# Kernel optimization log

Measured on AMD Instinct MI355X. Metric: run time of the kernel, lower is better.

## Reference

```python
import jax, jax.numpy as jnp
import numpy as np

NT, NF, CIN, COUT = 1_500_000, 500_000, 32, 32
BN_EPS = 1e-5


def setup_inputs() -> dict:
    key = jax.random.key(0)
    k1, k2, k3 = jax.random.split(key, 3)
    input_texture = jax.random.normal(k1, (NT, CIN), dtype=jnp.float32)
    # barycentric coefficients: nonnegative, rows sum to 1
    b = jax.random.uniform(k2, (NT, 3), dtype=jnp.float32) + 1e-3
    bary_coeff = b / b.sum(axis=1, keepdims=True)
    # 3 texture samples per facet (sum == NT)
    num_texture = jnp.full((NF,), 3, dtype=jnp.int32)
    # xavier-normal init for [Cout, Cin, 3] kernel
    fan = CIN * 3 + COUT * 3
    std = float(np.sqrt(2.0 / fan))
    weights = jax.random.normal(k3, (COUT, CIN, 3), dtype=jnp.float32) * std
    bias = jnp.zeros((1, COUT), dtype=jnp.float32)
    gamma = jnp.ones((COUT,), dtype=jnp.float32)
    beta = jnp.zeros((COUT,), dtype=jnp.float32)
    return {"input_texture": input_texture, "bary_coeff": bary_coeff,
            "num_texture": num_texture, "weights": weights, "bias": bias,
            "gamma": gamma, "beta": beta}


def reference(input_texture, bary_coeff, num_texture, weights, bias, gamma, beta):
    nf = num_texture.shape[0]
    nt = input_texture.shape[0]
    # segment id for each ragged texture sample (original op uses cumsum offsets)
    seg = jnp.repeat(jnp.arange(nf), num_texture, total_repeat_length=nt)
    # per-sample contribution: y[t,o] = sum_{c,k} x[t,c] * b[t,k] * W[o,c,k]
    y = jnp.einsum('tc,tk,ock->to', input_texture, bary_coeff, weights)
    # facet2facet averages over the samples of each facet
    s = jax.ops.segment_sum(y, seg, num_segments=nf)  # [Nf, Cout]
    cnt = jnp.maximum(num_texture.astype(y.dtype), 1)[:, None]
    out = s / cnt
    out = out + bias          # bias add
    out = jax.nn.relu(out)    # activation
    # BatchNorm1d in training mode: batch statistics over the facet dim
    mean = out.mean(axis=0)
    var = out.var(axis=0)
    out = (out - mean) * jax.lax.rsqrt(var + BN_EPS) * gamma + beta
    return out
```

## Files before the change

kernel.cpp:

```cpp
#include <hip/hip_runtime.h>
#include <hip/hip_bf16.h>
#include <stdint.h>

typedef __attribute__((ext_vector_type(4))) float fv4;
typedef __attribute__((ext_vector_type(4))) short sv4;
typedef __attribute__((ext_vector_type(8))) short sv8;

#define SCHUNK 2048
#define NIT 4
#define SPAN (64 * NIT)
#define PZB 108

static __device__ __forceinline__ short f2bf(float f) {
  __hip_bfloat16 h = __float2bfloat16(f);
  union { __hip_bfloat16 h; short s; } u; u.h = h;
  return u.s;
}

__global__ __launch_bounds__(256) void scan1(const int* __restrict__ num, int nf,
                                             int* __restrict__ bsum) {
  __shared__ int sd[256];
  int b = blockIdx.x, tid = threadIdx.x;
  int base = b * SCHUNK + tid * 8;
  int s = 0;
#pragma unroll
  for (int j = 0; j < 8; ++j) { int i = base + j; if (i < nf) s += num[i]; }
  sd[tid] = s; __syncthreads();
  for (int st = 128; st > 0; st >>= 1) {
    if (tid < st) sd[tid] += sd[tid + st];
    __syncthreads();
  }
  if (tid == 0) bsum[b] = sd[0];
}

__global__ __launch_bounds__(256) void scan2(int* __restrict__ bsum, int nb) {
  __shared__ int sd[256];
  int tid = threadIdx.x;
  int v = (tid < nb) ? bsum[tid] : 0;
  sd[tid] = v; __syncthreads();
  for (int off = 1; off < 256; off <<= 1) {
    int t = (tid >= off) ? sd[tid - off] : 0;
    __syncthreads();
    sd[tid] += t;
    __syncthreads();
  }
  if (tid < nb) bsum[tid] = sd[tid] - v;
}

__global__ __launch_bounds__(256) void scan3(const int* __restrict__ num, int nf,
                                             const int* __restrict__ bsum,
                                             int* __restrict__ offsets) {
  __shared__ int sc_[256];
  int b = blockIdx.x, tid = threadIdx.x;
  int base = b * SCHUNK + tid * 8;
  int loc[8]; int s = 0;
#pragma unroll
  for (int j = 0; j < 8; ++j) {
    loc[j] = (base + j < nf) ? num[base + j] : 0;
    s += loc[j];
  }
  sc_[tid] = s; __syncthreads();
  for (int off = 1; off < 256; off <<= 1) {
    int t = (tid >= off) ? sc_[tid - off] : 0;
    __syncthreads();
    sc_[tid] += t;
    __syncthreads();
  }
  int run = bsum[b] + sc_[tid] - s;
#pragma unroll
  for (int j = 0; j < 8; ++j) {
    if (base + j < nf) offsets[base + j] = run;
    run += loc[j];
  }
  if (b == gridDim.x - 1 && tid == 255) offsets[nf] = run;
}

__global__ __launch_bounds__(256) void k_main(
    const float* __restrict__ x, const float* __restrict__ bary,
    const float* __restrict__ W, const float* __restrict__ bias,
    const int* __restrict__ offsets, float* __restrict__ out,
    float* __restrict__ partials, int nf, int nt, int nw)
{
  __shared__ short W2[32 * PZB];
  __shared__ short Z[4 * 16 * PZB];

  const int tid = threadIdx.x;
  const int lane = tid & 63;
  const int wv = tid >> 6;
  short* Zw = &Z[wv * 16 * PZB];

  for (int idx = tid; idx < 3072; idx += 256) {
    int o = idx / 96;
    int ck = idx - o * 96;
    int k = ck >> 5, c = ck & 31;
    W2[o * PZB + ck] = f2bf(W[o * 96 + c * 3 + k]);
  }
  __syncthreads();

  const int fl = lane >> 2;
  const int cb = (lane & 3) * 8;
  const int rowl = lane & 15;
  const int grp = lane >> 4;
  const int blk0 = blockIdx.x * SPAN;

  float bo0 = bias[rowl];
  float bo1 = bias[16 + rowl];
  float s1l = 0.f, s1h = 0.f, s2l = 0.f, s2h = 0.f;

  for (int t = 0; t < NIT; ++t) {
    const int f0t = blk0 + t * 64 + wv * 16;
    const int f = f0t + fl;
    const int fa = f < nf ? f : nf;
    const int fb = (f + 1) < nf ? (f + 1) : nf;

    const int st = offsets[fa];
    const int en = offsets[fb];
    const int s3 = 3 * f;
    const int sbase = (f < nf && s3 + 3 <= nt) ? s3 : 0;
    const float* xp0 = x + (size_t)(sbase + 0) * 32 + cb;
    const float* xp1 = x + (size_t)(sbase + 1) * 32 + cb;
    const float* xp2 = x + (size_t)(sbase + 2) * 32 + cb;
    fv4 x0a = *(const fv4*)(xp0), x0b = *(const fv4*)(xp0 + 4);
    fv4 x1a = *(const fv4*)(xp1), x1b = *(const fv4*)(xp1 + 4);
    fv4 x2a = *(const fv4*)(xp2), x2b = *(const fv4*)(xp2 + 4);
    const float* bp0 = bary + (size_t)(sbase + 0) * 3;
    const float* bp1 = bary + (size_t)(sbase + 1) * 3;
    const float* bp2 = bary + (size_t)(sbase + 2) * 3;
    float b00 = bp0[0], b01 = bp0[1], b02 = bp0[2];
    float b10 = bp1[0], b11 = bp1[1], b12 = bp1[2];
    float b20 = bp2[0], b21 = bp2[1], b22 = bp2[2];

    const int nm_my = en - st;

    float z0[8], z1[8], z2[8];
#pragma unroll
    for (int j = 0; j < 8; ++j) { z0[j] = 0.f; z1[j] = 0.f; z2[j] = 0.f; }

    if (nm_my == 3 && st == s3) {
#pragma unroll
      for (int j = 0; j < 4; ++j) {
        z0[j]     += x0a[j] * b00; z1[j]     += x0a[j] * b01; z2[j]     += x0a[j] * b02;
        z0[4 + j] += x0b[j] * b00; z1[4 + j] += x0b[j] * b01; z2[4 + j] += x0b[j] * b02;
      }
#pragma unroll
      for (int j = 0; j < 4; ++j) {
        z0[j]     += x1a[j] * b10; z1[j]     += x1a[j] * b11; z2[j]     += x1a[j] * b12;
        z0[4 + j] += x1b[j] * b10; z1[4 + j] += x1b[j] * b11; z2[4 + j] += x1b[j] * b12;
      }
#pragma unroll
      for (int j = 0; j < 4; ++j) {
        z0[j]     += x2a[j] * b20; z1[j]     += x2a[j] * b21; z2[j]     += x2a[j] * b22;
        z0[4 + j] += x2b[j] * b20; z1[4 + j] += x2b[j] * b21; z2[4 + j] += x2b[j] * b22;
      }
    } else {
      for (int t2 = st; t2 < en; ++t2) {
        const float* xp = x + (size_t)t2 * 32 + cb;
        fv4 xa = *(const fv4*)(xp);
        fv4 xb = *(const fv4*)(xp + 4);
        const float* bp = bary + (size_t)t2 * 3;
        float b0 = bp[0], b1 = bp[1], b2 = bp[2];
#pragma unroll
        for (int j = 0; j < 4; ++j) {
          z0[j]     += xa[j] * b0; z1[j]     += xa[j] * b1; z2[j]     += xa[j] * b2;
          z0[4 + j] += xb[j] * b0; z1[4 + j] += xb[j] * b1; z2[4 + j] += xb[j] * b2;
        }
      }
    }

    short* zr = &Zw[fl * PZB + cb];
#pragma unroll
    for (int g = 0; g < 2; ++g) {
      sv4 p0, p1, p2;
#pragma unroll
      for (int j = 0; j < 4; ++j) {
        p0[j] = f2bf(z0[g * 4 + j]);
        p1[j] = f2bf(z1[g * 4 + j]);
        p2[j] = f2bf(z2[g * 4 + j]);
      }
      *(sv4*)(zr + g * 4)      = p0;
      *(sv4*)(zr + 32 + g * 4) = p1;
      *(sv4*)(zr + 64 + g * 4) = p2;
    }
    __builtin_amdgcn_wave_barrier();

    fv4 acc0 = (fv4){0.f, 0.f, 0.f, 0.f};
    fv4 acc1 = (fv4){0.f, 0.f, 0.f, 0.f};
#pragma unroll
    for (int kb = 0; kb < 3; ++kb) {
      const int cko = kb * 32 + grp * 4;
      sv8 bfr0, bfr1, afr;
      {
        const short* wr = &W2[rowl * PZB + cko];
        sv4 lo = *(const sv4*)(wr), hi = *(const sv4*)(wr + 16);
#pragma unroll
        for (int j = 0; j < 4; ++j) { bfr0[j] = lo[j]; bfr0[4 + j] = hi[j]; }
      }
      {
        const short* wr = &W2[(16 + rowl) * PZB + cko];
        sv4 lo = *(const sv4*)(wr), hi = *(const sv4*)(wr + 16);
#pragma unroll
        for (int j = 0; j < 4; ++j) { bfr1[j] = lo[j]; bfr1[4 + j] = hi[j]; }
      }
      {
        const short* zr2 = &Zw[rowl * PZB + cko];
        sv4 lo = *(const sv4*)(zr2), hi = *(const sv4*)(zr2 + 16);
#pragma unroll
        for (int j = 0; j < 4; ++j) { afr[j] = lo[j]; afr[4 + j] = hi[j]; }
      }
      acc0 = __builtin_amdgcn_mfma_f32_16x16x32_bf16(afr, bfr0, acc0, 0, 0, 0);
      acc1 = __builtin_amdgcn_mfma_f32_16x16x32_bf16(afr, bfr1, acc1, 0, 0, 0);
    }

#pragma unroll
    for (int r = 0; r < 4; ++r) {
      int row = grp * 4 + r;
      int fr = f0t + row;
      int nm = __shfl(nm_my, row * 4, 64);
      float inv = 1.0f / (float)(nm > 1 ? nm : 1);
      if (fr < nf) {
        float v0 = fmaxf(acc0[r] * inv + bo0, 0.f);
        float v1 = fmaxf(acc1[r] * inv + bo1, 0.f);
        out[fr * 32 + rowl]      = v0;
        out[fr * 32 + 16 + rowl] = v1;
        s1l += v0; s2l += v0 * v0;
        s1h += v1; s2h += v1 * v1;
      }
    }
    __builtin_amdgcn_wave_barrier();
  }

  s1l += __shfl_xor(s1l, 16, 64); s1l += __shfl_xor(s1l, 32, 64);
  s1h += __shfl_xor(s1h, 16, 64); s1h += __shfl_xor(s1h, 32, 64);
  s2l += __shfl_xor(s2l, 16, 64); s2l += __shfl_xor(s2l, 32, 64);
  s2h += __shfl_xor(s2h, 16, 64); s2h += __shfl_xor(s2h, 32, 64);
  if (grp == 0) {
    int w = blockIdx.x * 4 + wv;
    partials[(long)(rowl)      * nw + w] = s1l;
    partials[(long)(16 + rowl) * nw + w] = s1h;
    partials[(long)(32 + rowl) * nw + w] = s2l;
    partials[(long)(48 + rowl) * nw + w] = s2h;
  }
}

__global__ __launch_bounds__(256) void k_reduce(const float* __restrict__ partials,
                                                int nw, float* __restrict__ stats) {
  __shared__ float sd[256];
  int c = blockIdx.x;
  const float* p = partials + (long)c * nw;
  float s = 0.f;
  for (int i = threadIdx.x; i < nw; i += 256) s += p[i];
  sd[threadIdx.x] = s; __syncthreads();
  for (int st = 128; st > 0; st >>= 1) {
    if (threadIdx.x < st) sd[threadIdx.x] += sd[threadIdx.x + st];
    __syncthreads();
  }
  if (threadIdx.x == 0) stats[c] = sd[0];
}

__global__ __launch_bounds__(256) void k_bn(float* __restrict__ out,
                                            const float* __restrict__ stats,
                                            const float* __restrict__ gamma,
                                            const float* __restrict__ beta, int nf) {
  __shared__ float sc[32], sh[32];
  if (threadIdx.x < 32) {
    int o = threadIdx.x;
    float inv_n = 1.0f / (float)nf;
    float mean = stats[o] * inv_n;
    float var = stats[32 + o] * inv_n - mean * mean;
    float rstd = rsqrtf(var + 1e-5f);
    float g = gamma[o] * rstd;
    sc[o] = g;
    sh[o] = beta[o] - mean * g;
  }
  __syncthreads();
  long total4 = (long)nf * 8;
  long idx0 = (long)blockIdx.x * 256 + threadIdx.x;
  int ob = ((int)idx0 & 7) * 4;
  fv4 scv = *(const fv4*)&sc[ob];
  fv4 shv = *(const fv4*)&sh[ob];
  for (long idx = idx0; idx < total4; idx += (long)gridDim.x * 256) {
    fv4 v = *((const fv4*)out + idx);
    v = v * scv + shv;
    *((fv4*)out + idx) = v;
  }
}

extern "C" void kernel_launch(void* const* d_in, const int* in_sizes, int n_in,
                              void* d_out, int out_size, void* d_ws, size_t ws_size,
                              hipStream_t stream) {
  const float* x     = (const float*)d_in[0];
  const float* bary  = (const float*)d_in[1];
  const int*   numt  = (const int*)d_in[2];
  const float* W     = (const float*)d_in[3];
  const float* bias  = (const float*)d_in[4];
  const float* gamma = (const float*)d_in[5];
  const float* beta  = (const float*)d_in[6];
  float* out = (float*)d_out;

  const int nf   = in_sizes[2];
  const int nt   = in_sizes[0] / 32;
  const int nblk = (nf + SPAN - 1) / SPAN;
  const int nw   = nblk * 4;
  const int nbS  = (nf + SCHUNK - 1) / SCHUNK;

  char* w = (char*)d_ws;
  int* offsets = (int*)w;
  size_t off1 = (4UL * (size_t)(nf + 1) + 255) & ~255UL;
  int* bsum = (int*)(w + off1);
  size_t off2 = (off1 + 4UL * (size_t)nbS + 255) & ~255UL;
  float* partials = (float*)(w + off2);
  size_t off3 = (off2 + 4UL * 64UL * (size_t)nw + 255) & ~255UL;
  float* stats = (float*)(w + off3);

  scan1<<<nbS, 256, 0, stream>>>(numt, nf, bsum);
  scan2<<<1, 256, 0, stream>>>(bsum, nbS);
  scan3<<<nbS, 256, 0, stream>>>(numt, nf, bsum, offsets);
  k_main<<<nblk, 256, 0, stream>>>(x, bary, W, bias, offsets, out, partials, nf, nt, nw);
  k_reduce<<<64, 256, 0, stream>>>(partials, nw, stats);
  k_bn<<<2048, 256, 0, stream>>>(out, stats, gamma, beta, nf);
}
```

Baseline: 97.81 us.

## Double-buffer global loads across iterations in k_main via register sets

Restructures the per-wave loop so the global loads of x, bary and offsets for the next 64-facet tile are issued into a second register set before the current tile is computed. This software pipelining is meant to hide global memory latency behind the FMA, LDS and MFMA work of the previous tile. It roughly doubles the live registers for loaded data, which may lower occupancy, and the compiler may already have been overlapping these loads.

```diff
diff --git a/kernel.cpp b/kernel.cpp
--- a/kernel.cpp
+++ b/kernel.cpp
@@ -75,6 +75,130 @@
   if (b == gridDim.x - 1 && tid == 255) offsets[nf] = run;
 }
 
+#define DECL_SET(S) \
+  int st_##S, en_##S; \
+  fv4 x0a_##S, x0b_##S, x1a_##S, x1b_##S, x2a_##S, x2b_##S; \
+  float b00_##S, b01_##S, b02_##S, b10_##S, b11_##S, b12_##S, b20_##S, b21_##S, b22_##S;
+
+#define LOAD_SET(S, T) do { \
+  const int f_ = blk0 + (T) * 64 + wv * 16 + fl; \
+  const int fa_ = f_ < nf ? f_ : nf; \
+  const int fb_ = (f_ + 1) < nf ? (f_ + 1) : nf; \
+  st_##S = offsets[fa_]; \
+  en_##S = offsets[fb_]; \
+  const int s3_ = 3 * f_; \
+  const int sbase_ = (f_ < nf && s3_ + 3 <= nt) ? s3_ : 0; \
+  const float* xp0_ = x + (size_t)(sbase_ + 0) * 32 + cb; \
+  const float* xp1_ = x + (size_t)(sbase_ + 1) * 32 + cb; \
+  const float* xp2_ = x + (size_t)(sbase_ + 2) * 32 + cb; \
+  x0a_##S = *(const fv4*)(xp0_); x0b_##S = *(const fv4*)(xp0_ + 4); \
+  x1a_##S = *(const fv4*)(xp1_); x1b_##S = *(const fv4*)(xp1_ + 4); \
+  x2a_##S = *(const fv4*)(xp2_); x2b_##S = *(const fv4*)(xp2_ + 4); \
+  const float* bp0_ = bary + (size_t)(sbase_ + 0) * 3; \
+  const float* bp1_ = bary + (size_t)(sbase_ + 1) * 3; \
+  const float* bp2_ = bary + (size_t)(sbase_ + 2) * 3; \
+  b00_##S = bp0_[0]; b01_##S = bp0_[1]; b02_##S = bp0_[2]; \
+  b10_##S = bp1_[0]; b11_##S = bp1_[1]; b12_##S = bp1_[2]; \
+  b20_##S = bp2_[0]; b21_##S = bp2_[1]; b22_##S = bp2_[2]; \
+} while (0)
+
+#define COMPUTE_SET(S, T) do { \
+  const int f0t = blk0 + (T) * 64 + wv * 16; \
+  const int f_ = f0t + fl; \
+  const int nm_my = en_##S - st_##S; \
+  float z0[8], z1[8], z2[8]; \
+  _Pragma("unroll") \
+  for (int j = 0; j < 8; ++j) { z0[j] = 0.f; z1[j] = 0.f; z2[j] = 0.f; } \
+  if (nm_my == 3 && st_##S == 3 * f_) { \
+    _Pragma("unroll") \
+    for (int j = 0; j < 4; ++j) { \
+      z0[j]     += x0a_##S[j] * b00_##S; z1[j]     += x0a_##S[j] * b01_##S; z2[j]     += x0a_##S[j] * b02_##S; \
+      z0[4 + j] += x0b_##S[j] * b00_##S; z1[4 + j] += x0b_##S[j] * b01_##S; z2[4 + j] += x0b_##S[j] * b02_##S; \
+    } \
+    _Pragma("unroll") \
+    for (int j = 0; j < 4; ++j) { \
+      z0[j]     += x1a_##S[j] * b10_##S; z1[j]     += x1a_##S[j] * b11_##S; z2[j]     += x1a_##S[j] * b12_##S; \
+      z0[4 + j] += x1b_##S[j] * b10_##S; z1[4 + j] += x1b_##S[j] * b11_##S; z2[4 + j] += x1b_##S[j] * b12_##S; \
+    } \
+    _Pragma("unroll") \
+    for (int j = 0; j < 4; ++j) { \
+      z0[j]     += x2a_##S[j] * b20_##S; z1[j]     += x2a_##S[j] * b21_##S; z2[j]     += x2a_##S[j] * b22_##S; \
+      z0[4 + j] += x2b_##S[j] * b20_##S; z1[4 + j] += x2b_##S[j] * b21_##S; z2[4 + j] += x2b_##S[j] * b22_##S; \
+    } \
+  } else { \
+    for (int t2 = st_##S; t2 < en_##S; ++t2) { \
+      const float* xp_ = x + (size_t)t2 * 32 + cb; \
+      fv4 xa_ = *(const fv4*)(xp_); \
+      fv4 xb_ = *(const fv4*)(xp_ + 4); \
+      const float* bp_ = bary + (size_t)t2 * 3; \
+      float b0_ = bp_[0], b1_ = bp_[1], b2_ = bp_[2]; \
+      _Pragma("unroll") \
+      for (int j = 0; j < 4; ++j) { \
+        z0[j]     += xa_[j] * b0_; z1[j]     += xa_[j] * b1_; z2[j]     += xa_[j] * b2_; \
+        z0[4 + j] += xb_[j] * b0_; z1[4 + j] += xb_[j] * b1_; z2[4 + j] += xb_[j] * b2_; \
+      } \
+    } \
+  } \
+  short* zr_ = &Zw[fl * PZB + cb]; \
+  _Pragma("unroll") \
+  for (int g = 0; g < 2; ++g) { \
+    sv4 p0_, p1_, p2_; \
+    _Pragma("unroll") \
+    for (int j = 0; j < 4; ++j) { \
+      p0_[j] = f2bf(z0[g * 4 + j]); \
+      p1_[j] = f2bf(z1[g * 4 + j]); \
+      p2_[j] = f2bf(z2[g * 4 + j]); \
+    } \
+    *(sv4*)(zr_ + g * 4)      = p0_; \
+    *(sv4*)(zr_ + 32 + g * 4) = p1_; \
+    *(sv4*)(zr_ + 64 + g * 4) = p2_; \
+  } \
+  __builtin_amdgcn_wave_barrier(); \
+  fv4 acc0 = (fv4){0.f, 0.f, 0.f, 0.f}; \
+  fv4 acc1 = (fv4){0.f, 0.f, 0.f, 0.f}; \
+  _Pragma("unroll") \
+  for (int kb = 0; kb < 3; ++kb) { \
+    const int cko = kb * 32 + grp * 4; \
+    sv8 bfr0, bfr1, afr; \
+    { \
+      const short* wr_ = &W2[rowl * PZB + cko]; \
+      sv4 lo_ = *(const sv4*)(wr_), hi_ = *(const sv4*)(wr_ + 16); \
+      _Pragma("unroll") \
+      for (int j = 0; j < 4; ++j) { bfr0[j] = lo_[j]; bfr0[4 + j] = hi_[j]; } \
+    } \
+    { \
+      const short* wr_ = &W2[(16 + rowl) * PZB + cko]; \
+      sv4 lo_ = *(const sv4*)(wr_), hi_ = *(const sv4*)(wr_ + 16); \
+      _Pragma("unroll") \
+      for (int j = 0; j < 4; ++j) { bfr1[j] = lo_[j]; bfr1[4 + j] = hi_[j]; } \
+    } \
+    { \
+      const short* zr2_ = &Zw[rowl * PZB + cko]; \
+      sv4 lo_ = *(const sv4*)(zr2_), hi_ = *(const sv4*)(zr2_ + 16); \
+      _Pragma("unroll") \
+      for (int j = 0; j < 4; ++j) { afr[j] = lo_[j]; afr[4 + j] = hi_[j]; } \
+    } \
+    acc0 = __builtin_amdgcn_mfma_f32_16x16x32_bf16(afr, bfr0, acc0, 0, 0, 0); \
+    acc1 = __builtin_amdgcn_mfma_f32_16x16x32_bf16(afr, bfr1, acc1, 0, 0, 0); \
+  } \
+  _Pragma("unroll") \
+  for (int r = 0; r < 4; ++r) { \
+    int row_ = grp * 4 + r; \
+    int fr_ = f0t + row_; \
+    int nm_ = __shfl(nm_my, row_ * 4, 64); \
+    float inv_ = 1.0f / (float)(nm_ > 1 ? nm_ : 1); \
+    if (fr_ < nf) { \
+      float v0_ = fmaxf(acc0[r] * inv_ + bo0, 0.f); \
+      float v1_ = fmaxf(acc1[r] * inv_ + bo1, 0.f); \
+      out[fr_ * 32 + rowl]      = v0_; \
+      out[fr_ * 32 + 16 + rowl] = v1_; \
+      s1l += v0_; s2l += v0_ * v0_; \
+      s1h += v1_; s2h += v1_ * v1_; \
+    } \
+  } \
+  __builtin_amdgcn_wave_barrier(); \
+} while (0)
+
 __global__ __launch_bounds__(256) void k_main(
     const float* __restrict__ x, const float* __restrict__ bary,
     const float* __restrict__ W, const float* __restrict__ bias,
@@ -107,126 +231,17 @@
   float bo1 = bias[16 + rowl];
   float s1l = 0.f, s1h = 0.f, s2l = 0.f, s2h = 0.f;
 
-  for (int t = 0; t < NIT; ++t) {
-    const int f0t = blk0 + t * 64 + wv * 16;
-    const int f = f0t + fl;
-    const int fa = f < nf ? f : nf;
-    const int fb = (f + 1) < nf ? (f + 1) : nf;
-
-    const int st = offsets[fa];
-    const int en = offsets[fb];
-    const int s3 = 3 * f;
-    const int sbase = (f < nf && s3 + 3 <= nt) ? s3 : 0;
-    const float* xp0 = x + (size_t)(sbase + 0) * 32 + cb;
-    const float* xp1 = x + (size_t)(sbase + 1) * 32 + cb;
-    const float* xp2 = x + (size_t)(sbase + 2) * 32 + cb;
-    fv4 x0a = *(const fv4*)(xp0), x0b = *(const fv4*)(xp0 + 4);
-    fv4 x1a = *(const fv4*)(xp1), x1b = *(const fv4*)(xp1 + 4);
-    fv4 x2a = *(const fv4*)(xp2), x2b = *(const fv4*)(xp2 + 4);
-    const float* bp0 = bary + (size_t)(sbase + 0) * 3;
-    const float* bp1 = bary + (size_t)(sbase + 1) * 3;
-    const float* bp2 = bary + (size_t)(sbase + 2) * 3;
-    float b00 = bp0[0], b01 = bp0[1], b02 = bp0[2];
-    float b10 = bp1[0], b11 = bp1[1], b12 = bp1[2];
-    float b20 = bp2[0], b21 = bp2[1], b22 = bp2[2];
-
-    const int nm_my = en - st;
-
-    float z0[8], z1[8], z2[8];
+  DECL_SET(A)
+  DECL_SET(B)
+
+  LOAD_SET(A, 0);
 #pragma unroll
-    for (int j = 0; j < 8; ++j) { z0[j] = 0.f; z1[j] = 0.f; z2[j] = 0.f; }
-
-    if (nm_my == 3 && st == s3) {
-#pragma unroll
-      for (int j = 0; j < 4; ++j) {
-        z0[j]     += x0a[j] * b00; z1[j]     += x0a[j] * b01; z2[j]     += x0a[j] * b02;
-        z0[4 + j] += x0b[j] * b00; z1[4 + j] += x0b[j] * b01; z2[4 + j] += x0b[j] * b02;
-      }
-#pragma unroll
-      for (int j = 0; j < 4; ++j) {
-        z0[j]     += x1a[j] * b10; z1[j]     += x1a[j] * b11; z2[j]     += x1a[j] * b12;
-        z0[4 + j] += x1b[j] * b10; z1[4 + j] += x1b[j] * b11; z2[4 + j] += x1b[j] * b12;
-      }
-#pragma unroll
-      for (int j = 0; j < 4; ++j) {
-        z0[j]     += x2a[j] * b20; z1[j]     += x2a[j] * b21; z2[j]     += x2a[j] * b22;
-        z0[4 + j] += x2b[j] * b20; z1[4 + j] += x2b[j] * b21; z2[4 + j] += x2b[j] * b22;
-      }
-    } else {
-      for (int t2 = st; t2 < en; ++t2) {
-        const float* xp = x + (size_t)t2 * 32 + cb;
-        fv4 xa = *(const fv4*)(xp);
-        fv4 xb = *(const fv4*)(xp + 4);
-        const float* bp = bary + (size_t)t2 * 3;
-        float b0 = bp[0], b1 = bp[1], b2 = bp[2];
-#pragma unroll
-        for (int j = 0; j < 4; ++j) {
-          z0[j]     += xa[j] * b0; z1[j]     += xa[j] * b1; z2[j]     += xa[j] * b2;
-          z0[4 + j] += xb[j] * b0; z1[4 + j] += xb[j] * b1; z2[4 + j] += xb[j] * b2;
-        }
-      }
-    }
-
-    short* zr = &Zw[fl * PZB + cb];
-#pragma unroll
-    for (int g = 0; g < 2; ++g) {
-      sv4 p0, p1, p2;
-#pragma unroll
-      for (int j = 0; j < 4; ++j) {
-        p0[j] = f2bf(z0[g * 4 + j]);
-        p1[j] = f2bf(z1[g * 4 + j]);
-        p2[j] = f2bf(z2[g * 4 + j]);
-      }
-      *(sv4*)(zr + g * 4)      = p0;
-      *(sv4*)(zr + 32 + g * 4) = p1;
-      *(sv4*)(zr + 64 + g * 4) = p2;
-    }
-    __builtin_amdgcn_wave_barrier();
-
-    fv4 acc0 = (fv4){0.f, 0.f, 0.f, 0.f};
-    fv4 acc1 = (fv4){0.f, 0.f, 0.f, 0.f};
-#pragma unroll
-    for (int kb = 0; kb < 3; ++kb) {
-      const int cko = kb * 32 + grp * 4;
-      sv8 bfr0, bfr1, afr;
-      {
-        const short* wr = &W2[rowl * PZB + cko];
-        sv4 lo = *(const sv4*)(wr), hi = *(const sv4*)(wr + 16);
-#pragma unroll
-        for (int j = 0; j < 4; ++j) { bfr0[j] = lo[j]; bfr0[4 + j] = hi[j]; }
-      }
-      {
-        const short* wr = &W2[(16 + rowl) * PZB + cko];
-        sv4 lo = *(const sv4*)(wr), hi = *(const sv4*)(wr + 16);
-#pragma unroll
-        for (int j = 0; j < 4; ++j) { bfr1[j] = lo[j]; bfr1[4 + j] = hi[j]; }
-      }
-      {
-        const short* zr2 = &Zw[rowl * PZB + cko];
-        sv4 lo = *(const sv4*)(zr2), hi = *(const sv4*)(zr2 + 16);
-#pragma unroll
-        for (int j = 0; j < 4; ++j) { afr[j] = lo[j]; afr[4 + j] = hi[j]; }
-      }
-      acc0 = __builtin_amdgcn_mfma_f32_16x16x32_bf16(afr, bfr0, acc0, 0, 0, 0);
-      acc1 = __builtin_amdgcn_mfma_f32_16x16x32_bf16(afr, bfr1, acc1, 0, 0, 0);
-    }
-
-#pragma unroll
-    for (int r = 0; r < 4; ++r) {
-      int row = grp * 4 + r;
-      int fr = f0t + row;
-      int nm = __shfl(nm_my, row * 4, 64);
-      float inv = 1.0f / (float)(nm > 1 ? nm : 1);
-      if (fr < nf) {
-        float v0 = fmaxf(acc0[r] * inv + bo0, 0.f);
-        float v1 = fmaxf(acc1[r] * inv + bo1, 0.f);
-        out[fr * 32 + rowl]      = v0;
-        out[fr * 32 + 16 + rowl] = v1;
-        s1l += v0; s2l += v0 * v0;
-        s1h += v1; s2h += v1 * v1;
-      }
-    }
-    __builtin_amdgcn_wave_barrier();
+  for (int tt = 0; tt < NIT / 2; ++tt) {
+    const int t0 = 2 * tt, t1 = 2 * tt + 1;
+    LOAD_SET(B, t1);
+    COMPUTE_SET(A, t0);
+    if (t1 + 1 < NIT) LOAD_SET(A, t1 + 1);
+    COMPUTE_SET(B, t1);
   }
 
   s1l += __shfl_xor(s1l, 16, 64); s1l += __shfl_xor(s1l, 32, 64);
```

New measurement: 97.04 us. Within noise of the previous version (-0.8%).

## Feed MFMA A operand directly from registers, hoist weight fragments

Applied to the files above, without the earlier changes.

Remaps the per-lane work so each lane computes the bary-weighted features for its MFMA row and column group, letting the A fragment be built in registers instead of round-tripping through LDS. Weight B fragments are loaded from shared memory once before the loop, and the facet loop is unrolled. This removes the LDS stores, loads and wave barriers per iteration, at the cost of more registers and less contiguous per-lane x loads (two separated 16-byte chunks per row).

```diff
diff --git a/kernel.cpp b/kernel.cpp
--- a/kernel.cpp
+++ b/kernel.cpp
@@ -82,12 +82,10 @@
     float* __restrict__ partials, int nf, int nt, int nw)
 {
   __shared__ short W2[32 * PZB];
-  __shared__ short Z[4 * 16 * PZB];
 
   const int tid = threadIdx.x;
   const int lane = tid & 63;
   const int wv = tid >> 6;
-  short* Zw = &Z[wv * 16 * PZB];
 
   for (int idx = tid; idx < 3072; idx += 256) {
     int o = idx / 96;
@@ -97,19 +95,38 @@
   }
   __syncthreads();
 
-  const int fl = lane >> 2;
-  const int cb = (lane & 3) * 8;
   const int rowl = lane & 15;
   const int grp = lane >> 4;
+  const int cb_lo = grp * 4;
+  const int cb_hi = grp * 4 + 16;
   const int blk0 = blockIdx.x * SPAN;
+
+  sv8 bfrA[3], bfrB[3];
+#pragma unroll
+  for (int kb = 0; kb < 3; ++kb) {
+    const int cko = kb * 32 + grp * 4;
+    {
+      const short* wr = &W2[rowl * PZB + cko];
+      sv4 lo = *(const sv4*)(wr), hi = *(const sv4*)(wr + 16);
+#pragma unroll
+      for (int j = 0; j < 4; ++j) { bfrA[kb][j] = lo[j]; bfrA[kb][4 + j] = hi[j]; }
+    }
+    {
+      const short* wr = &W2[(16 + rowl) * PZB + cko];
+      sv4 lo = *(const sv4*)(wr), hi = *(const sv4*)(wr + 16);
+#pragma unroll
+      for (int j = 0; j < 4; ++j) { bfrB[kb][j] = lo[j]; bfrB[kb][4 + j] = hi[j]; }
+    }
+  }
 
   float bo0 = bias[rowl];
   float bo1 = bias[16 + rowl];
   float s1l = 0.f, s1h = 0.f, s2l = 0.f, s2h = 0.f;
 
+#pragma unroll
   for (int t = 0; t < NIT; ++t) {
     const int f0t = blk0 + t * 64 + wv * 16;
-    const int f = f0t + fl;
+    const int f = f0t + rowl;
     const int fa = f < nf ? f : nf;
     const int fb = (f + 1) < nf ? (f + 1) : nf;
 
@@ -117,12 +134,12 @@
     const int en = offsets[fb];
     const int s3 = 3 * f;
     const int sbase = (f < nf && s3 + 3 <= nt) ? s3 : 0;
-    const float* xp0 = x + (size_t)(sbase + 0) * 32 + cb;
-    const float* xp1 = x + (size_t)(sbase + 1) * 32 + cb;
-    const float* xp2 = x + (size_t)(sbase + 2) * 32 + cb;
-    fv4 x0a = *(const fv4*)(xp0), x0b = *(const fv4*)(xp0 + 4);
-    fv4 x1a = *(const fv4*)(xp1), x1b = *(const fv4*)(xp1 + 4);
-    fv4 x2a = *(const fv4*)(xp2), x2b = *(const fv4*)(xp2 + 4);
+    const float* xp0 = x + (size_t)(sbase + 0) * 32;
+    const float* xp1 = x + (size_t)(sbase + 1) * 32;
+    const float* xp2 = x + (size_t)(sbase + 2) * 32;
+    fv4 x0a = *(const fv4*)(xp0 + cb_lo), x0b = *(const fv4*)(xp0 + cb_hi);
+    fv4 x1a = *(const fv4*)(xp1 + cb_lo), x1b = *(const fv4*)(xp1 + cb_hi);
+    fv4 x2a = *(const fv4*)(xp2 + cb_lo), x2b = *(const fv4*)(xp2 + cb_hi);
     const float* bp0 = bary + (size_t)(sbase + 0) * 3;
     const float* bp1 = bary + (size_t)(sbase + 1) * 3;
     const float* bp2 = bary + (size_t)(sbase + 2) * 3;
@@ -154,9 +171,9 @@
       }
     } else {
       for (int t2 = st; t2 < en; ++t2) {
-        const float* xp = x + (size_t)t2 * 32 + cb;
-        fv4 xa = *(const fv4*)(xp);
-        fv4 xb = *(const fv4*)(xp + 4);
+        const float* xp = x + (size_t)t2 * 32;
+        fv4 xa = *(const fv4*)(xp + cb_lo);
+        fv4 xb = *(const fv4*)(xp + cb_hi);
         const float* bp = bary + (size_t)t2 * 3;
         float b0 = bp[0], b1 = bp[1], b2 = bp[2];
 #pragma unroll
@@ -167,55 +184,27 @@
       }
     }
 
-    short* zr = &Zw[fl * PZB + cb];
-#pragma unroll
-    for (int g = 0; g < 2; ++g) {
-      sv4 p0, p1, p2;
-#pragma unroll
-      for (int j = 0; j < 4; ++j) {
-        p0[j] = f2bf(z0[g * 4 + j]);
-        p1[j] = f2bf(z1[g * 4 + j]);
-        p2[j] = f2bf(z2[g * 4 + j]);
-      }
-      *(sv4*)(zr + g * 4)      = p0;
-      *(sv4*)(zr + 32 + g * 4) = p1;
-      *(sv4*)(zr + 64 + g * 4) = p2;
-    }
-    __builtin_amdgcn_wave_barrier();
-
     fv4 acc0 = (fv4){0.f, 0.f, 0.f, 0.f};
     fv4 acc1 = (fv4){0.f, 0.f, 0.f, 0.f};
 #pragma unroll
     for (int kb = 0; kb < 3; ++kb) {
-      const int cko = kb * 32 + grp * 4;
-      sv8 bfr0, bfr1, afr;
-      {
-        const short* wr = &W2[rowl * PZB + cko];
-        sv4 lo = *(const sv4*)(wr), hi = *(const sv4*)(wr + 16);
-#pragma unroll
-        for (int j = 0; j < 4; ++j) { bfr0[j] = lo[j]; bfr0[4 + j] = hi[j]; }
-      }
-      {
-        const short* wr = &W2[(16 + rowl) * PZB + cko];
-        sv4 lo = *(const sv4*)(wr), hi = *(const sv4*)(wr + 16);
-#pragma unroll
-        for (int j = 0; j < 4; ++j) { bfr1[j] = lo[j]; bfr1[4 + j] = hi[j]; }
-      }
-      {
-        const short* zr2 = &Zw[rowl * PZB + cko];
-        sv4 lo = *(const sv4*)(zr2), hi = *(const sv4*)(zr2 + 16);
-#pragma unroll
-        for (int j = 0; j < 4; ++j) { afr[j] = lo[j]; afr[4 + j] = hi[j]; }
-      }
-      acc0 = __builtin_amdgcn_mfma_f32_16x16x32_bf16(afr, bfr0, acc0, 0, 0, 0);
-      acc1 = __builtin_amdgcn_mfma_f32_16x16x32_bf16(afr, bfr1, acc1, 0, 0, 0);
+      sv8 afr;
+#pragma unroll
+      for (int j = 0; j < 4; ++j) {
+        float lo = (kb == 0) ? z0[j]     : (kb == 1) ? z1[j]     : z2[j];
+        float hi = (kb == 0) ? z0[4 + j] : (kb == 1) ? z1[4 + j] : z2[4 + j];
+        afr[j]     = f2bf(lo);
+        afr[4 + j] = f2bf(hi);
+      }
+      acc0 = __builtin_amdgcn_mfma_f32_16x16x32_bf16(afr, bfrA[kb], acc0, 0, 0, 0);
+      acc1 = __builtin_amdgcn_mfma_f32_16x16x32_bf16(afr, bfrB[kb], acc1, 0, 0, 0);
     }
 
 #pragma unroll
     for (int r = 0; r < 4; ++r) {
       int row = grp * 4 + r;
       int fr = f0t + row;
-      int nm = __shfl(nm_my, row * 4, 64);
+      int nm = __shfl(nm_my, row, 64);
       float inv = 1.0f / (float)(nm > 1 ? nm : 1);
       if (fr < nf) {
         float v0 = fmaxf(acc0[r] * inv + bo0, 0.f);
@@ -226,7 +215,6 @@
         s1h += v1; s2h += v1 * v1;
       }
     }
-    __builtin_amdgcn_wave_barrier();
   }
 
   s1l += __shfl_xor(s1l, 16, 64); s1l += __shfl_xor(s1l, 32, 64);
```

Result: slower. 103.7 us (+6.1%).
